# Kernel tuning notes

Hardware: AMD Instinct MI355X
Metric: run time of the kernel (lower is better)

The kernel has to match this reference:

```python
import jax, jax.numpy as jnp
import numpy as np
from jax import lax

B, M = 8192, 200
OUT_W = OUT_H = 16
NUM_LAYERS = 32
CNN_CH = 64
FLAT = CNN_CH * 2 * 2  # conv5/s3: 16->4, conv3/s1: 4->2
INPUT_SIZE = 128
HIDDEN = 128
CRITIC_H = 1024
ACTOR_H = 512
EMB_D = 16
NUM_ACTIONS = 100


def setup_inputs() -> dict:
    key = jax.random.key(0)
    ks = jax.random.split(key, 20)
    # token observations: [coord_byte, attr_index, attr_value] packed as int32
    coords = jax.random.randint(ks[0], (B, M), 0, 256)          # coord byte; 255 = invalid token
    attrs = jax.random.randint(ks[1], (B, M), 0, 40)            # some >= NUM_LAYERS -> masked
    vals = jax.random.randint(ks[2], (B, M), 0, 256)
    observations = jnp.stack([coords, attrs, vals], axis=-1).astype(jnp.int32)

    def lin(k, out_d, in_d, scale=None):
        s = scale if scale is not None else 1.0 / np.sqrt(in_d)
        return jax.random.uniform(k, (out_d, in_d), jnp.float32, -s, s)

    max_vec = jax.random.uniform(ks[3], (1, NUM_LAYERS, 1, 1), jnp.float32, 0.5, 30.0)
    cnn1_w = jax.random.normal(ks[4], (CNN_CH, NUM_LAYERS, 5, 5), jnp.float32) * 0.05
    cnn1_b = jnp.zeros((CNN_CH,), jnp.float32)
    cnn2_w = jax.random.normal(ks[5], (CNN_CH, CNN_CH, 3, 3), jnp.float32) * 0.05
    cnn2_b = jnp.zeros((CNN_CH,), jnp.float32)
    fc1_w = lin(ks[6], 128, FLAT); fc1_b = jnp.zeros((128,), jnp.float32)
    enc_w = lin(ks[7], INPUT_SIZE, 128); enc_b = jnp.zeros((INPUT_SIZE,), jnp.float32)
    critic1_w = lin(ks[8], CRITIC_H, HIDDEN); critic1_b = jnp.zeros((CRITIC_H,), jnp.float32)
    value_w = lin(ks[9], 1, CRITIC_H); value_b = jnp.zeros((1,), jnp.float32)
    actor1_w = lin(ks[10], ACTOR_H, HIDDEN); actor1_b = jnp.zeros((ACTOR_H,), jnp.float32)
    emb = jax.random.normal(ks[11], (NUM_ACTIONS, EMB_D), jnp.float32)
    action_emb = emb * (0.1 / jnp.max(jnp.abs(emb)))
    bound = 1.0 / np.sqrt(ACTOR_H)
    actor_W = jax.random.uniform(ks[12], (1, ACTOR_H, EMB_D), jnp.float32, -bound, bound)
    actor_bias = jax.random.uniform(ks[13], (1,), jnp.float32, -bound, bound)
    return dict(observations=observations, max_vec=max_vec,
                cnn1_w=cnn1_w, cnn1_b=cnn1_b, cnn2_w=cnn2_w, cnn2_b=cnn2_b,
                fc1_w=fc1_w, fc1_b=fc1_b, enc_w=enc_w, enc_b=enc_b,
                critic1_w=critic1_w, critic1_b=critic1_b, value_w=value_w, value_b=value_b,
                actor1_w=actor1_w, actor1_b=actor1_b, action_emb=action_emb,
                actor_W=actor_W, actor_bias=actor_bias)


def _encode_box(observations):
    # bit-unpack coord byte, mask, scatter into dense [B, L, W, H] box
    coords = observations[..., 0]                       # [B, M]
    x_idx = (coords >> 4) & 15
    y_idx = coords & 15
    atr_idx = observations[..., 1]
    atr_val = observations[..., 2].astype(jnp.float32)
    valid = (coords != 255) & (atr_idx < NUM_LAYERS)
    dim = OUT_W * OUT_H
    combined = atr_idx * dim + x_idx * OUT_H + y_idx    # [B, M]
    safe_idx = jnp.where(valid, combined, 0)
    safe_val = jnp.where(valid, atr_val, 0.0)
    box = jnp.zeros((observations.shape[0], NUM_LAYERS * dim), jnp.float32)
    box = box.at[jnp.arange(observations.shape[0])[:, None], safe_idx].set(safe_val)
    return box.reshape(-1, NUM_LAYERS, OUT_W, OUT_H)


def _conv(x, w, b, stride):
    y = lax.conv_general_dilated(x, w, (stride, stride), 'VALID',
                                 dimension_numbers=('NCHW', 'OIHW', 'NCHW'))
    return y + b[None, :, None, None]


def reference(observations, max_vec, cnn1_w, cnn1_b, cnn2_w, cnn2_b, fc1_w, fc1_b,
              enc_w, enc_b, critic1_w, critic1_b, value_w, value_b,
              actor1_w, actor1_b, action_emb, actor_W, actor_bias):
    box = _encode_box(observations)
    x = box / max_vec
    x = jax.nn.relu(_conv(x, cnn1_w, cnn1_b, 3))
    x = jax.nn.relu(_conv(x, cnn2_w, cnn2_b, 1))
    x = x.reshape(x.shape[0], -1)                       # [B, FLAT]
    x = jax.nn.relu(x @ fc1_w.T + fc1_b)
    hidden = jax.nn.relu(x @ enc_w.T + enc_b)           # [B, 128]
    # critic
    cf = jnp.tanh(hidden @ critic1_w.T + critic1_b)
    value = cf @ value_w.T + value_b                    # [B, 1]
    # bilinear actor (k=1: query is action-independent)
    af = jax.nn.relu(hidden @ actor1_w.T + actor1_b)    # [B, ACTOR_H]
    query = jnp.tanh(jnp.einsum('bh,he->be', af, actor_W[0]))
    logits = query @ action_emb[:NUM_ACTIONS].T + actor_bias  # [B, NUM_ACTIONS]
    return logits, value
```

## Files before the change

### kernel.cpp

```cpp
#include <hip/hip_runtime.h>
#include <math.h>

#define B_ 8192

typedef __attribute__((ext_vector_type(8))) short short8;
typedef __attribute__((ext_vector_type(4))) float f32x4;

__device__ unsigned short g_w1p[51200];
__device__ unsigned short g_w2p[36864];
__device__ unsigned short g_fc1hi[32768], g_fc1lo[32768];
__device__ unsigned short g_enchi[16384], g_enclo[16384];
__device__ unsigned short g_crp[131072];
__device__ unsigned short g_acp[65536];
__device__ unsigned short g_qWp[8192];
__device__ unsigned short g_ACT1hi[8192*1024];

__device__ __forceinline__ unsigned short f2bf(float v){
    unsigned u = __builtin_bit_cast(unsigned, v);
    unsigned r = (u + 0x7fffu + ((u >> 16) & 1u)) >> 16;
    return (unsigned short)r;
}
__device__ __forceinline__ float bf2f(unsigned short h){
    unsigned u = ((unsigned)h) << 16;
    return __builtin_bit_cast(float, u);
}
__device__ __forceinline__ void split_store(float v, unsigned short* hi, unsigned short* lo){
    unsigned short h = f2bf(v);
    *hi = h;
    *lo = f2bf(v - bf2f(h));
}

__global__ __launch_bounds__(256) void prep_kernel(
    const float* __restrict__ w1, const float* __restrict__ maxv,
    const float* __restrict__ w2, const float* __restrict__ fc1,
    const float* __restrict__ enc, const float* __restrict__ cr,
    const float* __restrict__ ac, const float* __restrict__ aW)
{
    int d = blockIdx.x * 256 + threadIdx.x;
    if (d < 51200){
        int n = d / 800, k = d - n*800;
        int l = k / 25;
        float v = w1[d] / maxv[l];
        int kc = k >> 5, kh = k & 31, ng = n >> 4, r = n & 15;
        int idx = ((kc*4 + ng)*16 + r)*32 + kh;
        g_w1p[idx] = f2bf(v);
        return;
    }
    d -= 51200;
    if (d < 36864){
        int oc = d / 576, k2 = d - oc*576;
        int kxy = k2 >> 6, ic = k2 & 63;
        float v = w2[oc*576 + ic*9 + kxy];
        int kc = k2 >> 6, ks = (k2 >> 5) & 1, kq = k2 & 31, nt = oc >> 4, r = oc & 15;
        int idx = (((kc*2 + ks)*4 + nt)*16 + r)*32 + kq;
        g_w2p[idx] = f2bf(v);
        return;
    }
    d -= 36864;
    if (d < 32768){
        int n = d >> 8, kp = d & 255;
        float v = fc1[n*256 + (kp & 63)*4 + (kp >> 6)];
        int idx = ((((n >> 4)*8) + (kp >> 5))*16 + (n & 15))*32 + (kp & 31);
        split_store(v, &g_fc1hi[idx], &g_fc1lo[idx]);
        return;
    }
    d -= 32768;
    if (d < 16384){
        int n = d >> 7, k = d & 127;
        int idx = ((((n >> 4)*4) + (k >> 5))*16 + (n & 15))*32 + (k & 31);
        split_store(enc[d], &g_enchi[idx], &g_enclo[idx]);
        return;
    }
    d -= 16384;
    if (d < 131072){
        int n = d >> 7, k = d & 127;
        int idx = ((((n >> 4)*4) + (k >> 5))*16 + (n & 15))*32 + (k & 31);
        g_crp[idx] = f2bf(cr[d]);
        return;
    }
    d -= 131072;
    if (d < 65536){
        int n = d >> 7, k = d & 127;
        int idx = ((((n >> 4)*4) + (k >> 5))*16 + (n & 15))*32 + (k & 31);
        g_acp[idx] = f2bf(ac[d]);
        return;
    }
    d -= 65536;
    {
        int e = d >> 9, j = d & 511;
        int idx = ((j >> 5)*16 + e)*32 + (j & 31);
        g_qWp[idx] = f2bf(aW[j*16 + e]);
    }
}

#define APITCH 808
__global__ __launch_bounds__(256) void conv1_kernel(const int* __restrict__ obs,
                                                    const float* __restrict__ b1)
{
    const int b = blockIdx.x;
    const int tid = threadIdx.x;
    const int wave = tid >> 6, lane = tid & 63;
    const int l15 = lane & 15, lhi = lane >> 4;

    __shared__ unsigned short sA[32 * APITCH];
    int* wtab = (int*)sA;

    const unsigned short* Bh = &g_w1p[wave*512 + l15*32 + lhi*8];
    short8 bh0 = *(const short8*)&Bh[0*2048];
    short8 bh1 = *(const short8*)&Bh[1*2048];
    short8 bh2 = *(const short8*)&Bh[2*2048];
    short8 bh3 = *(const short8*)&Bh[3*2048];

    int   cells[2], xs[2], ys[2], ls[2];
    float vals[2];
    bool  valids[2], kept[2];
    #pragma unroll
    for (int u = 0; u < 2; u++){
        const int slot = tid + u*256;
        valids[u] = false; kept[u] = false; cells[u] = 0;
        if (slot < 400){
            const int si = (slot >= 200) ? 1 : 0;
            const int k  = slot - si*200;
            const int base = (b*2 + si)*600 + k*3;
            int coord = obs[base], atr = obs[base+1], val = obs[base+2];
            bool valid = (coord != 255) && (atr < 32);
            xs[u] = (coord >> 4) & 15;  ys[u] = coord & 15;  ls[u] = atr;
            cells[u] = valid ? (atr*256 + xs[u]*16 + ys[u]) : 0;
            vals[u]  = (float)val;
            valids[u] = valid;
        }
    }
    if (tid < 200) wtab[cells[0]] = -1;
    __syncthreads();
    if (tid < 200) atomicMax(&wtab[cells[0]], tid);
    __syncthreads();
    if (tid < 200) kept[0] = (wtab[cells[0]] == tid);
    __syncthreads();
    if (tid >= 200) wtab[cells[0]] = -1;
    if (tid < 144)  wtab[cells[1]] = -1;
    __syncthreads();
    if (tid >= 200) atomicMax(&wtab[cells[0]], tid - 200);
    if (tid < 144)  atomicMax(&wtab[cells[1]], tid + 56);
    __syncthreads();
    if (tid >= 200) kept[0] = (wtab[cells[0]] == tid - 200);
    if (tid < 144)  kept[1] = (wtab[cells[1]] == tid + 56);
    __syncthreads();

    for (int i = tid; i < 4 * APITCH; i += 256)
        *(short8*)&sA[i * 8] = short8{0,0,0,0,0,0,0,0};
    __syncthreads();

    #pragma unroll
    for (int u = 0; u < 2; u++){
        const int slot = tid + u*256;
        if (slot < 400 && kept[u] && valids[u]){
            const int si = (slot >= 200) ? 1 : 0;
            const int x3 = xs[u]/3, rx = xs[u] - 3*x3;
            const int y3 = ys[u]/3, ry = ys[u] - 3*y3;
            const unsigned short hv = f2bf(vals[u]);
            #pragma unroll
            for (int d = 0; d < 4; d++){
                const int dxd = d >> 1, dyd = d & 1;
                const int ox = x3 - dxd, oy = y3 - dyd;
                const int wx = rx + 3*dxd, wy = ry + 3*dyd;
                if (((unsigned)ox <= 3u) && ((unsigned)oy <= 3u) && (wx < 5) && (wy < 5))
                    sA[(si*16 + ox*4 + oy)*APITCH + ls[u]*25 + wx*5 + wy] = hv;
            }
        }
    }
    __syncthreads();

    const int n = wave*16 + l15;
    const unsigned short* A0 = &sA[l15*APITCH + lhi*8];
    const unsigned short* A1 = &sA[(16 + l15)*APITCH + lhi*8];
    f32x4 acc0e = {0,0,0,0}, acc1e = {0,0,0,0};
    f32x4 acc0o = {0,0,0,0}, acc1o = {0,0,0,0};
    #pragma unroll
    for (int kc2 = 0; kc2 < 12; kc2++){
        const int kc = kc2*2;
        short8 a0e = *(const short8*)&A0[kc*32];
        short8 a1e = *(const short8*)&A1[kc*32];
        short8 a0o = *(const short8*)&A0[(kc+1)*32];
        short8 a1o = *(const short8*)&A1[(kc+1)*32];
        short8 bhn0, bhn1;
        if (kc2 < 10){
            bhn0 = *(const short8*)&Bh[(kc + 4)*2048];
            bhn1 = *(const short8*)&Bh[(kc + 5)*2048];
        } else if (kc2 == 10){
            bhn0 = *(const short8*)&Bh[24*2048];
        }
        acc0e = __builtin_amdgcn_mfma_f32_16x16x32_bf16(a0e, bh0, acc0e, 0, 0, 0);
        acc1e = __builtin_amdgcn_mfma_f32_16x16x32_bf16(a1e, bh0, acc1e, 0, 0, 0);
        acc0o = __builtin_amdgcn_mfma_f32_16x16x32_bf16(a0o, bh1, acc0o, 0, 0, 0);
        acc1o = __builtin_amdgcn_mfma_f32_16x16x32_bf16(a1o, bh1, acc1o, 0, 0, 0);
        bh0 = bh2; bh1 = bh3; bh2 = bhn0; bh3 = bhn1;
    }
    {
        short8 a0e = *(const short8*)&A0[24*32];
        short8 a1e = *(const short8*)&A1[24*32];
        acc0e = __builtin_amdgcn_mfma_f32_16x16x32_bf16(a0e, bh0, acc0e, 0, 0, 0);
        acc1e = __builtin_amdgcn_mfma_f32_16x16x32_bf16(a1e, bh0, acc1e, 0, 0, 0);
    }
    f32x4 acc0, acc1;
    #pragma unroll
    for (int j = 0; j < 4; j++){ acc0[j] = acc0e[j] + acc0o[j]; acc1[j] = acc1e[j] + acc1o[j]; }

    const float bb = b1[n];
    #pragma unroll
    for (int j = 0; j < 4; j++){
        const int pos = lhi*4 + j;
        float v0 = fmaxf(acc0[j] + bb, 0.f);
        float v1 = fmaxf(acc1[j] + bb, 0.f);
        g_ACT1hi[(b*2    )*1024 + pos*64 + n] = f2bf(v0);
        g_ACT1hi[(b*2 + 1)*1024 + pos*64 + n] = f2bf(v1);
    }
}

__global__ __launch_bounds__(512, 4) void tail_kernel(
    const float* __restrict__ b2,   const float* __restrict__ fc1b,
    const float* __restrict__ encb, const float* __restrict__ crb,
    const float* __restrict__ vw,   const float* __restrict__ vb,
    const float* __restrict__ acb,  const float* __restrict__ emb,
    const float* __restrict__ abias, float* __restrict__ out)
{
    const int r0 = blockIdx.x * 16;
    const int tid = threadIdx.x, wave = tid >> 6, lane = tid & 63;
    const int l15 = lane & 15, lhi = lane >> 4;
    const int coff = l15*32 + lhi*8;

    __shared__ char smem[52736];
    unsigned short* sA1h = (unsigned short*)smem;
    unsigned short* sA1l = (unsigned short*)(smem + 8448);
    float*          qpart= (float*)smem;
    unsigned short* sXh  = (unsigned short*)(smem + 16896);
    unsigned short* sXl  = (unsigned short*)(smem + 21248);
    float* svred = (float*)(smem + 16896);
    float* sq    = (float*)(smem + 17408);
    float* semb  = (float*)(smem + 18496);
    unsigned short* sHh  = (unsigned short*)(smem + 25600);
    unsigned short* sHl  = (unsigned short*)(smem + 29952);
    unsigned short* cb   = (unsigned short*)(smem + 34304);

    {
        unsigned short* sAh = cb;
        f32x4 c2acc[2] = {{0,0,0,0},{0,0,0,0}};
        const int srow = tid >> 3, sch8 = (tid & 7) * 8;
        const int spx = (srow >> 1) & 1, spy = srow & 1;
        const int sbase = (r0 + (srow >> 2))*1024;
        for (int kc = 0; kc < 9; kc++){
            const int kx = kc / 3, ky = kc - 3*kx;
            __syncthreads();
            {
                const int cell = (spx + kx)*4 + (spy + ky);
                *(short8*)&sAh[srow*72 + sch8] = *(const short8*)&g_ACT1hi[sbase + cell*64 + sch8];
            }
            __syncthreads();
            #pragma unroll
            for (int wt = 0; wt < 2; wt++){
                const int tile = wave*2 + wt, mt = tile >> 2, nt = tile & 3;
                #pragma unroll
                for (int ks = 0; ks < 2; ks++){
                    const int kk = ks*32 + lhi*8;
                    short8 a = *(const short8*)&sAh[(mt*16 + l15)*72 + kk];
                    const int t = (kc*2 + ks)*4 + nt;
                    const short8 bh = *(const short8*)&g_w2p[t*512 + coff];
                    c2acc[wt] = __builtin_amdgcn_mfma_f32_16x16x32_bf16(a, bh, c2acc[wt], 0, 0, 0);
                }
            }
        }
        __syncthreads();
        #pragma unroll
        for (int wt = 0; wt < 2; wt++){
            const int tile = wave*2 + wt, mt = tile >> 2, nt = tile & 3;
            const int col = nt*16 + l15;
            const float bb = b2[col];
            #pragma unroll
            for (int j = 0; j < 4; j++){
                const int row = mt*16 + lhi*4 + j;
                float v = fmaxf(c2acc[wt][j] + bb, 0.f);
                unsigned short h = f2bf(v);
                const int ai = (row >> 2)*264 + (row & 3)*64 + col;
                sA1h[ai] = h;
                sA1l[ai] = f2bf(v - bf2f(h));
            }
        }
    }
    __syncthreads();

    {
        f32x4 acc = {0,0,0,0};
        const int n = wave*16 + l15;
        #pragma unroll
        for (int kk8 = 0; kk8 < 8; kk8++){
            const int kk = kk8*32 + lhi*8;
            short8 ah = *(const short8*)&sA1h[l15*264 + kk];
            short8 al = *(const short8*)&sA1l[l15*264 + kk];
            const short8 bh = *(const short8*)&g_fc1hi[(wave*8 + kk8)*512 + coff];
            const short8 bl = *(const short8*)&g_fc1lo[(wave*8 + kk8)*512 + coff];
            acc = __builtin_amdgcn_mfma_f32_16x16x32_bf16(ah, bh, acc, 0, 0, 0);
            acc = __builtin_amdgcn_mfma_f32_16x16x32_bf16(al, bh, acc, 0, 0, 0);
            acc = __builtin_amdgcn_mfma_f32_16x16x32_bf16(ah, bl, acc, 0, 0, 0);
        }
        __syncthreads();
        const float bb = fc1b[n];
        #pragma unroll
        for (int j = 0; j < 4; j++){
            const int row = lhi*4 + j;
            float v = fmaxf(acc[j] + bb, 0.f);
            unsigned short h = f2bf(v);
            sXh[row*136 + n] = h;
            sXl[row*136 + n] = f2bf(v - bf2f(h));
        }
    }
    __syncthreads();

    {
        f32x4 acc = {0,0,0,0};
        const int n = wave*16 + l15;
        #pragma unroll
        for (int kk4 = 0; kk4 < 4; kk4++){
            const int kk = kk4*32 + lhi*8;
            short8 ah = *(const short8*)&sXh[l15*136 + kk];
            short8 al = *(const short8*)&sXl[l15*136 + kk];
            const short8 bh = *(const short8*)&g_enchi[(wave*4 + kk4)*512 + coff];
            const short8 bl = *(const short8*)&g_enclo[(wave*4 + kk4)*512 + coff];
            acc = __builtin_amdgcn_mfma_f32_16x16x32_bf16(ah, bh, acc, 0, 0, 0);
            acc = __builtin_amdgcn_mfma_f32_16x16x32_bf16(al, bh, acc, 0, 0, 0);
            acc = __builtin_amdgcn_mfma_f32_16x16x32_bf16(ah, bl, acc, 0, 0, 0);
        }
        const float bb = encb[n];
        #pragma unroll
        for (int j = 0; j < 4; j++){
            const int row = lhi*4 + j;
            float v = fmaxf(acc[j] + bb, 0.f);
            unsigned short h = f2bf(v);
            sHh[row*136 + n] = h;
            sHl[row*136 + n] = f2bf(v - bf2f(h));
        }
    }
    __syncthreads();

    short8 Ah[4], Al[4];
    #pragma unroll
    for (int kk4 = 0; kk4 < 4; kk4++){
        const int kk = kk4*32 + lhi*8;
        Ah[kk4] = *(const short8*)&sHh[l15*136 + kk];
        Al[kk4] = *(const short8*)&sHl[l15*136 + kk];
    }

    {
        float vp[4] = {0,0,0,0};
        #pragma unroll
        for (int ntc = 0; ntc < 2; ntc++){
            f32x4 cacc[4];
            #pragma unroll
            for (int q = 0; q < 4; q++) cacc[q] = f32x4{0,0,0,0};
            #pragma unroll
            for (int q = 0; q < 4; q++){
                const int t = wave*8 + ntc*4 + q;
                #pragma unroll
                for (int kk4 = 0; kk4 < 4; kk4++){
                    const short8 bh = *(const short8*)&g_crp[(t*4 + kk4)*512 + coff];
                    cacc[q] = __builtin_amdgcn_mfma_f32_16x16x32_bf16(Ah[kk4], bh, cacc[q], 0, 0, 0);
                    cacc[q] = __builtin_amdgcn_mfma_f32_16x16x32_bf16(Al[kk4], bh, cacc[q], 0, 0, 0);
                }
            }
            #pragma unroll
            for (int q = 0; q < 4; q++){
                const int n = wave*128 + (ntc*4 + q)*16 + l15;
                const float w = vw[n], bb = crb[n];
                #pragma unroll
                for (int j = 0; j < 4; j++)
                    vp[j] += tanhf(cacc[q][j] + bb) * w;
            }
        }
        #pragma unroll
        for (int m = 1; m < 16; m <<= 1)
            #pragma unroll
            for (int j = 0; j < 4; j++) vp[j] += __shfl_xor(vp[j], m, 64);
        if (l15 == 0){
            #pragma unroll
            for (int j = 0; j < 4; j++)
                svred[wave*16 + lhi*4 + j] = vp[j];
        }
    }

    __syncthreads();
    f32x4 qacc = {0,0,0,0};
    {
        const int c = wave;
        f32x4 aacc[4];
        #pragma unroll
        for (int nt = 0; nt < 4; nt++) aacc[nt] = f32x4{0,0,0,0};
        #pragma unroll
        for (int kk4 = 0; kk4 < 4; kk4++){
            #pragma unroll
            for (int nt = 0; nt < 4; nt++){
                const int t = c*4 + nt;
                const short8 bh = *(const short8*)&g_acp[(t*4 + kk4)*512 + coff];
                aacc[nt] = __builtin_amdgcn_mfma_f32_16x16x32_bf16(Ah[kk4], bh, aacc[nt], 0, 0, 0);
                aacc[nt] = __builtin_amdgcn_mfma_f32_16x16x32_bf16(Al[kk4], bh, aacc[nt], 0, 0, 0);
            }
        }
        #pragma unroll
        for (int nt = 0; nt < 4; nt++){
            const int col = nt*16 + l15;
            const float bb = acb[c*64 + col];
            #pragma unroll
            for (int j = 0; j < 4; j++){
                const int row = lhi*4 + j;
                cb[(wave*16 + row)*72 + col] = f2bf(fmaxf(aacc[nt][j] + bb, 0.f));
            }
        }
        #pragma unroll
        for (int kk2 = 0; kk2 < 2; kk2++){
            const int kk = kk2*32 + lhi*8;
            const short8 qbh = *(const short8*)&g_qWp[(c*2 + kk2)*512 + coff];
            const short8 qah = *(const short8*)&cb[(wave*16 + l15)*72 + kk];
            qacc = __builtin_amdgcn_mfma_f32_16x16x32_bf16(qah, qbh, qacc, 0, 0, 0);
        }
    }
    #pragma unroll
    for (int j = 0; j < 4; j++)
        qpart[wave*256 + (lhi*4 + j)*16 + l15] = qacc[j];
    __syncthreads();

    if (tid < 16){
        float s = vb[0];
        #pragma unroll
        for (int w = 0; w < 8; w++) s += svred[w*16 + tid];
        out[B_*100 + r0 + tid] = s;
    }
    if (tid < 256){
        int row = tid >> 4, e = tid & 15;
        float s = 0.f;
        #pragma unroll
        for (int w = 0; w < 8; w++) s += qpart[w*256 + row*16 + e];
        sq[row*17 + e] = tanhf(s);
    }
    for (int k = tid; k < 1600; k += 512) semb[k] = emb[k];
    __syncthreads();
    for (int i = tid; i < 1600; i += 512){
        int row = i / 100, a = i - row*100;
        float s = abias[0];
        #pragma unroll
        for (int e = 0; e < 16; e++) s += sq[row*17 + e] * semb[a*16 + e];
        out[(r0 + row)*100 + a] = s;
    }
}

extern "C" void kernel_launch(void* const* d_in, const int* in_sizes, int n_in,
                              void* d_out, int out_size, void* d_ws, size_t ws_size,
                              hipStream_t stream) {
    const int*   obs   = (const int*)  d_in[0];
    const float* maxv  = (const float*)d_in[1];
    const float* w1    = (const float*)d_in[2];
    const float* b1    = (const float*)d_in[3];
    const float* w2    = (const float*)d_in[4];
    const float* b2    = (const float*)d_in[5];
    const float* fc1w  = (const float*)d_in[6];
    const float* fc1b  = (const float*)d_in[7];
    const float* encw  = (const float*)d_in[8];
    const float* encb  = (const float*)d_in[9];
    const float* crw   = (const float*)d_in[10];
    const float* crb   = (const float*)d_in[11];
    const float* vw    = (const float*)d_in[12];
    const float* vb    = (const float*)d_in[13];
    const float* acw   = (const float*)d_in[14];
    const float* acb   = (const float*)d_in[15];
    const float* emb   = (const float*)d_in[16];
    const float* aW    = (const float*)d_in[17];
    const float* abias = (const float*)d_in[18];
    float* out = (float*)d_out;

    prep_kernel<<<1336, 256, 0, stream>>>(w1, maxv, w2, fc1w, encw, crw, acw, aW);
    conv1_kernel<<<B_/2, 256, 0, stream>>>(obs, b1);
    tail_kernel<<<512, 512, 0, stream>>>(b2, fc1b, encb, crb, vw, vb, acb, emb, abias, out);
}
```

Before: 81.12 us.

## Stage full conv1 activation tile in LDS once for conv2 im2col

Instead of reloading a gathered 64-row im2col slice from global memory into shared memory for each of the 9 kernel positions, with two barriers per step, the block now loads all 16 samples' conv1 activations (16x1024 bf16, padded rows) into shared memory once. Each wave then indexes the im2col patch directly from that tile. The conv2 loop is fully unrolled with interleaved MFMAs for the two tiles. This removes 18 barriers and the repeated global gathers, at the cost of a larger LDS footprint overlapping other buffers.

```diff
diff --git a/kernel.cpp b/kernel.cpp
--- a/kernel.cpp
+++ b/kernel.cpp
@@ -240,32 +240,34 @@
     unsigned short* sHh  = (unsigned short*)(smem + 25600);
     unsigned short* sHl  = (unsigned short*)(smem + 29952);
     unsigned short* cb   = (unsigned short*)(smem + 34304);
-
-    {
-        unsigned short* sAh = cb;
+    unsigned short* sACT = (unsigned short*)(smem + 16896);
+
+    {
+        for (int u = tid; u < 2048; u += 512){
+            const int row = u >> 7, c8 = (u & 127) * 8;
+            *(short8*)&sACT[row*1032 + c8] = *(const short8*)&g_ACT1hi[(r0 + row)*1024 + c8];
+        }
+        __syncthreads();
+
         f32x4 c2acc[2] = {{0,0,0,0},{0,0,0,0}};
-        const int srow = tid >> 3, sch8 = (tid & 7) * 8;
-        const int spx = (srow >> 1) & 1, spy = srow & 1;
-        const int sbase = (r0 + (srow >> 2))*1024;
+        const int tile0 = wave*2,     mt0 = tile0 >> 2, nt0 = tile0 & 3;
+        const int tile1 = wave*2 + 1, mt1 = tile1 >> 2, nt1 = tile1 & 3;
+        const int row0 = mt0*16 + l15, smp0 = row0 >> 2, px0 = (row0 >> 1) & 1, py0 = row0 & 1;
+        const int row1 = mt1*16 + l15, smp1 = row1 >> 2, px1 = (row1 >> 1) & 1, py1 = row1 & 1;
+        #pragma unroll
         for (int kc = 0; kc < 9; kc++){
             const int kx = kc / 3, ky = kc - 3*kx;
-            __syncthreads();
-            {
-                const int cell = (spx + kx)*4 + (spy + ky);
-                *(short8*)&sAh[srow*72 + sch8] = *(const short8*)&g_ACT1hi[sbase + cell*64 + sch8];
-            }
-            __syncthreads();
-            #pragma unroll
-            for (int wt = 0; wt < 2; wt++){
-                const int tile = wave*2 + wt, mt = tile >> 2, nt = tile & 3;
-                #pragma unroll
-                for (int ks = 0; ks < 2; ks++){
-                    const int kk = ks*32 + lhi*8;
-                    short8 a = *(const short8*)&sAh[(mt*16 + l15)*72 + kk];
-                    const int t = (kc*2 + ks)*4 + nt;
-                    const short8 bh = *(const short8*)&g_w2p[t*512 + coff];
-                    c2acc[wt] = __builtin_amdgcn_mfma_f32_16x16x32_bf16(a, bh, c2acc[wt], 0, 0, 0);
-                }
+            const int cell0 = (px0 + kx)*4 + (py0 + ky);
+            const int cell1 = (px1 + kx)*4 + (py1 + ky);
+            #pragma unroll
+            for (int ks = 0; ks < 2; ks++){
+                const int kk = ks*32 + lhi*8;
+                short8 a0 = *(const short8*)&sACT[smp0*1032 + cell0*64 + kk];
+                short8 a1 = *(const short8*)&sACT[smp1*1032 + cell1*64 + kk];
+                const short8 b0 = *(const short8*)&g_w2p[((kc*2 + ks)*4 + nt0)*512 + coff];
+                const short8 b1 = *(const short8*)&g_w2p[((kc*2 + ks)*4 + nt1)*512 + coff];
+                c2acc[0] = __builtin_amdgcn_mfma_f32_16x16x32_bf16(a0, b0, c2acc[0], 0, 0, 0);
+                c2acc[1] = __builtin_amdgcn_mfma_f32_16x16x32_bf16(a1, b1, c2acc[1], 0, 0, 0);
             }
         }
         __syncthreads();
```

Measured after the change: 81.62 us. About the same (+0.6%).
